# Optimization experiments

Measured on AMD Instinct MI355X. Metric: run time of the kernel, lower is better.

## Reference

```python
import jax, jax.numpy as jnp
import numpy as np

N, E, R, B, DIN, H1, H2 = 50000, 1000000, 8, 30, 64, 64, 64


def setup_inputs() -> dict:
    key = jax.random.key(0)
    ks = jax.random.split(key, 12)
    node_features = jax.random.normal(ks[0], (N, DIN), dtype=jnp.float32)
    src = jax.random.randint(ks[1], (E,), 0, N)
    dst = jax.random.randint(ks[2], (E,), 0, N)
    edge_index = jnp.stack([src, dst]).astype(jnp.int64)
    edge_norm = jax.random.uniform(ks[3], (E,), dtype=jnp.float32)
    edge_type = jax.random.randint(ks[4], (E,), 0, R).astype(jnp.int64)
    s = 0.05  # param init scale
    basis = jax.random.normal(ks[5], (B, DIN, H1), dtype=jnp.float32) * s
    comp = jax.random.normal(ks[6], (R, B), dtype=jnp.float32) * s
    loop_weight = jax.random.normal(ks[7], (DIN, H1), dtype=jnp.float32) * s
    bias1 = jnp.zeros((H1,), dtype=jnp.float32)
    weight2 = jax.random.normal(ks[8], (H1, H2), dtype=jnp.float32) * s
    bias2 = jnp.zeros((H2,), dtype=jnp.float32)
    return dict(node_features=node_features, edge_index=edge_index,
                edge_norm=edge_norm, edge_type=edge_type, basis=basis,
                comp=comp, loop_weight=loop_weight, bias1=bias1,
                weight2=weight2, bias2=bias2)


def reference(node_features, edge_index, edge_norm, edge_type, basis, comp,
              loop_weight, bias1, weight2, bias2):
    n = node_features.shape[0]
    src, dst = edge_index[0], edge_index[1]

    # ---- RGCNConv (basis decomposition, sum aggregation, self-loop, bias) ----
    # relation weights from bases: [R, DIN, H1]
    Wrel = jnp.einsum('rb,bio->rio', comp, basis)
    # transform every node by every relation once: [N, R, H1]
    xr = jnp.einsum('ni,rio->nro', node_features, Wrel)
    # per-edge message via (src, edge_type) gather: [E, H1]
    msg = xr[src, edge_type]
    agg1 = jax.ops.segment_sum(msg, dst, num_segments=n)
    h = agg1 + node_features @ loop_weight + bias1

    # ---- GraphConv (symmetric 'both' normalization) ----
    ones = jnp.ones((src.shape[0],), dtype=h.dtype)
    deg_out = jnp.clip(jax.ops.segment_sum(ones, src, num_segments=n), 1.0, None)
    deg_in = jnp.clip(jax.ops.segment_sum(ones, dst, num_segments=n), 1.0, None)
    hs = h * jax.lax.rsqrt(deg_out)[:, None]
    agg2 = jax.ops.segment_sum(hs[src], dst, num_segments=n)
    agg2 = agg2 * jax.lax.rsqrt(deg_in)[:, None]
    out = agg2 @ weight2 + bias2
    return out
```

## Files before the change

### kernel.cpp

```cpp
#include <hip/hip_runtime.h>

#define N_NODES 50000
#define N_EDGES 1000000
#define NB      128
#define CHUNK   7813
#define NQ      8
#define QN      6256
#define NBLK2   196

#define A_PART    0
#define A_XR      0
#define A_Y2      0
#define A_DEGP    115200000
#define A_ROWPTR  115400000
#define A_BSUM    115600128
#define A_BBASE   115601024
#define A_CSR     115601920
#define A_HS      123601920
#define A_WALL    136401920

typedef unsigned int uint32;

__global__ void k_wall(const float* __restrict__ comp, const float* __restrict__ basis,
                       const float* __restrict__ loopw, float* __restrict__ Wall) {
    int idx = blockIdx.x * 256 + threadIdx.x;
    if (idx >= 9 * 4096) return;
    int r = idx >> 12, io = idx & 4095;
    float acc;
    if (r < 8) {
        acc = 0.f;
        #pragma unroll
        for (int b = 0; b < 30; ++b) acc += comp[r * 30 + b] * basis[b * 4096 + io];
    } else {
        acc = loopw[io];
    }
    Wall[idx] = acc;
}

__global__ __launch_bounds__(256) void k_hist2(const int* __restrict__ ei,
                                               uint32* __restrict__ part) {
    __shared__ __align__(16) uint32 h[QN];
    int t = threadIdx.x, b = blockIdx.x, q = blockIdx.y;
    int lo = q * QN;
    int nq = N_NODES - lo; if (nq > QN) nq = QN;
    int4* h4 = (int4*)h;
    for (int i = t; i < QN / 4; i += 256) h4[i] = make_int4(0, 0, 0, 0);
    __syncthreads();
    int e0 = b * CHUNK, e1 = e0 + CHUNK;
    if (e1 > N_EDGES) e1 = N_EDGES;
    for (int e = e0 + t; e < e1; e += 256) {
        int s = ei[e], d = ei[N_EDGES + e];
        unsigned rs = (unsigned)(s - lo), rd = (unsigned)(d - lo);
        if (rs < (unsigned)QN) atomicAdd(&h[rs], 1u);
        if (rd < (unsigned)QN) atomicAdd(&h[rd], 0x10000u);
    }
    __syncthreads();
    int4* d4 = (int4*)(part + b * N_NODES + lo);
    const int4* s4 = (const int4*)h;
    for (int i = t; i < nq / 4; i += 256) d4[i] = s4[i];
}

__global__ __launch_bounds__(256) void k_merge(const uint32* __restrict__ part,
                                               uint32* __restrict__ degp,
                                               int* __restrict__ bsum) {
    int t = threadIdx.x, v = blockIdx.x * 256 + t;
    uint32 s = 0;
    if (v < N_NODES) {
        #pragma unroll 8
        for (int b = 0; b < NB; ++b) s += part[b * N_NODES + v];
        degp[v] = s;
    }
    int din = (int)(s >> 16);
    int r = din;
    #pragma unroll
    for (int d = 1; d < 64; d <<= 1) r += __shfl_xor(r, d);
    __shared__ int wsum[4];
    int lane = t & 63, wid = t >> 6;
    if (lane == 0) wsum[wid] = r;
    __syncthreads();
    if (t == 0) bsum[blockIdx.x] = wsum[0] + wsum[1] + wsum[2] + wsum[3];
}

__global__ void k_scanb(const int* __restrict__ bsum, int* __restrict__ bbase) {
    int t = threadIdx.x;
    int v = (t < NBLK2) ? bsum[t] : 0;
    int lane = t & 63, wid = t >> 6;
    int x = v;
    #pragma unroll
    for (int d = 1; d < 64; d <<= 1) {
        int y = __shfl_up(x, d);
        if (lane >= d) x += y;
    }
    __shared__ int wsum[4];
    if (lane == 63) wsum[wid] = x;
    __syncthreads();
    int base = 0;
    for (int w = 0; w < wid; ++w) base += wsum[w];
    if (t < NBLK2) bbase[t] = base + x - v;
}

__global__ __launch_bounds__(256) void k_base(uint32* __restrict__ part,
                                              const uint32* __restrict__ degp,
                                              const int* __restrict__ bbase,
                                              int* __restrict__ rowptr) {
    int t = threadIdx.x, v = blockIdx.x * 256 + t;
    int din = (v < N_NODES) ? (int)(degp[v] >> 16) : 0;
    int lane = t & 63, wid = t >> 6;
    int x = din;
    #pragma unroll
    for (int d = 1; d < 64; d <<= 1) {
        int y = __shfl_up(x, d);
        if (lane >= d) x += y;
    }
    __shared__ int wsum[4];
    if (lane == 63) wsum[wid] = x;
    __syncthreads();
    int base = bbase[blockIdx.x];
    for (int w = 0; w < wid; ++w) base += wsum[w];
    int start = base + x - din;
    if (v < N_NODES) {
        rowptr[v] = start;
        if (v == N_NODES - 1) rowptr[N_NODES] = start + din;
        uint32 run = (uint32)start;
        for (int b = 0; b < NB; ++b) {
            uint32 p = part[b * N_NODES + v];
            part[b * N_NODES + v] = run;
            run += (p >> 16);
        }
    }
}

__global__ __launch_bounds__(256) void k_fill2(const int* __restrict__ ei,
                                               const int* __restrict__ etype,
                                               const uint32* __restrict__ fillbase,
                                               int2* __restrict__ csr) {
    __shared__ __align__(16) uint32 cur[QN];
    int t = threadIdx.x, b = blockIdx.x, q = blockIdx.y;
    int lo = q * QN;
    int nq = N_NODES - lo; if (nq > QN) nq = QN;
    const int4* s4 = (const int4*)(fillbase + b * N_NODES + lo);
    int4* c4 = (int4*)cur;
    for (int i = t; i < nq / 4; i += 256) c4[i] = s4[i];
    __syncthreads();
    int e0 = b * CHUNK, e1 = e0 + CHUNK;
    if (e1 > N_EDGES) e1 = N_EDGES;
    for (int e = e0 + t; e < e1; e += 256) {
        int d = ei[N_EDGES + e];
        unsigned rd = (unsigned)(d - lo);
        if (rd < (unsigned)QN) {
            int s = ei[e], ty = etype[e];
            uint32 pos = atomicAdd(&cur[rd], 1u);
            csr[pos] = make_int2(s * 9 + ty, s);
        }
    }
}

__global__ __launch_bounds__(256) void k_xr(const float* __restrict__ x,
                                            const float* __restrict__ Wall,
                                            float* __restrict__ xr) {
    __shared__ __align__(16) float At[32 * 256];
    __shared__ __align__(16) float Wt[32 * 64];
    int t = threadIdx.x;
    int n0 = blockIdx.x * 256;
    int r = blockIdx.y;
    int og = t & 7, ng = t >> 3;
    float acc[8][8];
    #pragma unroll
    for (int i = 0; i < 8; ++i)
        #pragma unroll
        for (int j = 0; j < 8; ++j) acc[i][j] = 0.f;

    #pragma unroll
    for (int ph = 0; ph < 2; ++ph) {
        if (ph) __syncthreads();
        #pragma unroll
        for (int j = 0; j < 8; ++j) {
            int f4 = t + j * 256;
            int n = f4 >> 3, k4 = f4 & 7;
            float4 v = make_float4(0.f, 0.f, 0.f, 0.f);
            if (n0 + n < N_NODES)
                v = *(const float4*)&x[(n0 + n) * 64 + ph * 32 + k4 * 4];
            int sl = n >> 2, nl = n & 3, kb = k4 * 4;
            At[(kb + 0) * 256 + (((sl ^ ((kb + 0) & 7)) << 2) | nl)] = v.x;
            At[(kb + 1) * 256 + (((sl ^ ((kb + 1) & 7)) << 2) | nl)] = v.y;
            At[(kb + 2) * 256 + (((sl ^ ((kb + 2) & 7)) << 2) | nl)] = v.z;
            At[(kb + 3) * 256 + (((sl ^ ((kb + 3) & 7)) << 2) | nl)] = v.w;
        }
        #pragma unroll
        for (int j = 0; j < 8; ++j) {
            int f = t + j * 256;
            Wt[f] = Wall[r * 4096 + ph * 2048 + f];
        }
        __syncthreads();
        #pragma unroll 4
        for (int k = 0; k < 32; ++k) {
            int c = k & 7;
            float4 aA = *(const float4*)&At[k * 256 + (((2 * ng) ^ c) << 2)];
            float4 aB = *(const float4*)&At[k * 256 + (((2 * ng + 1) ^ c) << 2)];
            float4 w0 = *(const float4*)&Wt[k * 64 + og * 8];
            float4 w1 = *(const float4*)&Wt[k * 64 + og * 8 + 4];
            float a_[8] = {aA.x, aA.y, aA.z, aA.w, aB.x, aB.y, aB.z, aB.w};
            float w_[8] = {w0.x, w0.y, w0.z, w0.w, w1.x, w1.y, w1.z, w1.w};
            #pragma unroll
            for (int i = 0; i < 8; ++i)
                #pragma unroll
                for (int j = 0; j < 8; ++j) acc[i][j] += a_[i] * w_[j];
        }
    }
    #pragma unroll
    for (int i = 0; i < 8; ++i) {
        int n = n0 + ng * 8 + i;
        if (n < N_NODES) {
            *(float4*)&xr[n * 576 + r * 64 + og * 8] =
                make_float4(acc[i][0], acc[i][1], acc[i][2], acc[i][3]);
            *(float4*)&xr[n * 576 + r * 64 + og * 8 + 4] =
                make_float4(acc[i][4], acc[i][5], acc[i][6], acc[i][7]);
        }
    }
}

__global__ __launch_bounds__(256) void k_agg1(const float* __restrict__ xr,
                                              const int2* __restrict__ csr,
                                              const int* __restrict__ rowptr,
                                              const uint32* __restrict__ degp,
                                              const float* __restrict__ bias1,
                                              float* __restrict__ hs) {
    int wid = threadIdx.x >> 6, lane = threadIdx.x & 63;
    int v = blockIdx.x * 4 + wid;
    if (v >= N_NODES) return;
    float acc = xr[(v * 9 + 8) * 64 + lane] + bias1[lane];
    int j = rowptr[v], end = rowptr[v + 1];
    for (; j + 4 <= end; j += 4) {
        int r0 = csr[j].x, r1 = csr[j + 1].x, r2 = csr[j + 2].x, r3 = csr[j + 3].x;
        float a0 = xr[r0 * 64 + lane], a1 = xr[r1 * 64 + lane];
        float a2 = xr[r2 * 64 + lane], a3 = xr[r3 * 64 + lane];
        acc += a0; acc += a1; acc += a2; acc += a3;
    }
    for (; j < end; ++j) acc += xr[csr[j].x * 64 + lane];
    float dg = (float)(degp[v] & 0xffffu);
    if (dg < 1.f) dg = 1.f;
    hs[v * 64 + lane] = acc * rsqrtf(dg);
}

__global__ __launch_bounds__(256) void k_agg2(const float* __restrict__ hs,
                                              const int2* __restrict__ csr,
                                              const int* __restrict__ rowptr,
                                              const uint32* __restrict__ degp,
                                              float* __restrict__ y2) {
    int wid = threadIdx.x >> 6, lane = threadIdx.x & 63;
    int v = blockIdx.x * 4 + wid;
    if (v >= N_NODES) return;
    float acc = 0.f;
    int j = rowptr[v], end = rowptr[v + 1];
    for (; j + 4 <= end; j += 4) {
        int r0 = csr[j].y, r1 = csr[j + 1].y, r2 = csr[j + 2].y, r3 = csr[j + 3].y;
        float a0 = hs[r0 * 64 + lane], a1 = hs[r1 * 64 + lane];
        float a2 = hs[r2 * 64 + lane], a3 = hs[r3 * 64 + lane];
        acc += a0; acc += a1; acc += a2; acc += a3;
    }
    for (; j < end; ++j) acc += hs[csr[j].y * 64 + lane];
    float dg = (float)(degp[v] >> 16);
    if (dg < 1.f) dg = 1.f;
    y2[v * 64 + lane] = acc * rsqrtf(dg);
}

__global__ __launch_bounds__(256) void k_gemm2(const float* __restrict__ y2,
                                               const float* __restrict__ w2,
                                               const float* __restrict__ bias2,
                                               float* __restrict__ out) {
    __shared__ __align__(16) float At[32 * 256];
    __shared__ __align__(16) float Wt[32 * 64];
    int t = threadIdx.x;
    int n0 = blockIdx.x * 256;
    int og = t & 7, ng = t >> 3;
    float acc[8][8];
    #pragma unroll
    for (int i = 0; i < 8; ++i)
        #pragma unroll
        for (int j = 0; j < 8; ++j) acc[i][j] = 0.f;

    #pragma unroll
    for (int ph = 0; ph < 2; ++ph) {
        if (ph) __syncthreads();
        #pragma unroll
        for (int j = 0; j < 8; ++j) {
            int f4 = t + j * 256;
            int n = f4 >> 3, k4 = f4 & 7;
            float4 v = make_float4(0.f, 0.f, 0.f, 0.f);
            if (n0 + n < N_NODES)
                v = *(const float4*)&y2[(n0 + n) * 64 + ph * 32 + k4 * 4];
            int sl = n >> 2, nl = n & 3, kb = k4 * 4;
            At[(kb + 0) * 256 + (((sl ^ ((kb + 0) & 7)) << 2) | nl)] = v.x;
            At[(kb + 1) * 256 + (((sl ^ ((kb + 1) & 7)) << 2) | nl)] = v.y;
            At[(kb + 2) * 256 + (((sl ^ ((kb + 2) & 7)) << 2) | nl)] = v.z;
            At[(kb + 3) * 256 + (((sl ^ ((kb + 3) & 7)) << 2) | nl)] = v.w;
        }
        #pragma unroll
        for (int j = 0; j < 8; ++j) {
            int f = t + j * 256;
            Wt[f] = w2[ph * 2048 + f];
        }
        __syncthreads();
        #pragma unroll 4
        for (int k = 0; k < 32; ++k) {
            int c = k & 7;
            float4 aA = *(const float4*)&At[k * 256 + (((2 * ng) ^ c) << 2)];
            float4 aB = *(const float4*)&At[k * 256 + (((2 * ng + 1) ^ c) << 2)];
            float4 w0 = *(const float4*)&Wt[k * 64 + og * 8];
            float4 w1 = *(const float4*)&Wt[k * 64 + og * 8 + 4];
            float a_[8] = {aA.x, aA.y, aA.z, aA.w, aB.x, aB.y, aB.z, aB.w};
            float w_[8] = {w0.x, w0.y, w0.z, w0.w, w1.x, w1.y, w1.z, w1.w};
            #pragma unroll
            for (int i = 0; i < 8; ++i)
                #pragma unroll
                for (int j = 0; j < 8; ++j) acc[i][j] += a_[i] * w_[j];
        }
    }
    float4 b0 = *(const float4*)&bias2[og * 8];
    float4 b1 = *(const float4*)&bias2[og * 8 + 4];
    #pragma unroll
    for (int i = 0; i < 8; ++i) {
        int n = n0 + ng * 8 + i;
        if (n < N_NODES) {
            *(float4*)&out[n * 64 + og * 8] =
                make_float4(acc[i][0] + b0.x, acc[i][1] + b0.y,
                            acc[i][2] + b0.z, acc[i][3] + b0.w);
            *(float4*)&out[n * 64 + og * 8 + 4] =
                make_float4(acc[i][4] + b1.x, acc[i][5] + b1.y,
                            acc[i][6] + b1.z, acc[i][7] + b1.w);
        }
    }
}

extern "C" void kernel_launch(void* const* d_in, const int* in_sizes, int n_in,
                              void* d_out, int out_size, void* d_ws, size_t ws_size,
                              hipStream_t stream) {
    const float* x      = (const float*)d_in[0];
    const int*   ei     = (const int*)d_in[1];
    const int*   etype  = (const int*)d_in[3];
    const float* basis  = (const float*)d_in[4];
    const float* comp   = (const float*)d_in[5];
    const float* loopw  = (const float*)d_in[6];
    const float* bias1  = (const float*)d_in[7];
    const float* w2     = (const float*)d_in[8];
    const float* bias2  = (const float*)d_in[9];
    float* out = (float*)d_out;

    char* ws = (char*)d_ws;
    uint32* part   = (uint32*)(ws + A_PART);
    float*  xr     = (float*)(ws + A_XR);
    float*  y2     = (float*)(ws + A_Y2);
    uint32* degp   = (uint32*)(ws + A_DEGP);
    int*    rowptr = (int*)(ws + A_ROWPTR);
    int*    bsum   = (int*)(ws + A_BSUM);
    int*    bbase  = (int*)(ws + A_BBASE);
    int2*   csr    = (int2*)(ws + A_CSR);
    float*  hs     = (float*)(ws + A_HS);
    float*  Wall   = (float*)(ws + A_WALL);

    k_wall<<<144, 256, 0, stream>>>(comp, basis, loopw, Wall);
    k_hist2<<<dim3(NB, NQ), 256, 0, stream>>>(ei, part);
    k_merge<<<NBLK2, 256, 0, stream>>>(part, degp, bsum);
    k_scanb<<<1, 256, 0, stream>>>(bsum, bbase);
    k_base<<<NBLK2, 256, 0, stream>>>(part, degp, bbase, rowptr);
    k_fill2<<<dim3(NB, NQ), 256, 0, stream>>>(ei, etype, part, csr);
    k_xr<<<dim3((N_NODES + 255) / 256, 9), 256, 0, stream>>>(x, Wall, xr);
    k_agg1<<<N_NODES / 4, 256, 0, stream>>>(xr, csr, rowptr, degp, bias1, hs);
    k_agg2<<<N_NODES / 4, 256, 0, stream>>>(hs, csr, rowptr, degp, y2);
    k_gemm2<<<(N_NODES + 255) / 256, 256, 0, stream>>>(y2, w2, bias2, out);
}
```

Baseline: 310.1 us.

## Replace partitioned LDS histogram CSR build with global-atomic counting and fill

The previous CSR build ran 128x8 blocks, each histogramming one edge chunk per node quarter in LDS, then merged and prefix-scanned 128 partial histograms per node. It now zeroes a degree array, counts degrees with one global atomic per edge endpoint, and fills the CSR with a global atomic cursor per destination node. This removes the eightfold re-reading of edges and the 128-way partial merge and scan traffic. In exchange it relies on contended global atomics, and the order of edges within each CSR row becomes nondeterministic, which changes the float summation order.

Result: slower. 417.9 us (+34.8%).

```diff
diff --git a/kernel.cpp b/kernel.cpp
--- a/kernel.cpp
+++ b/kernel.cpp
@@ -2,13 +2,10 @@
 
 #define N_NODES 50000
 #define N_EDGES 1000000
-#define NB      128
-#define CHUNK   7813
-#define NQ      8
-#define QN      6256
 #define NBLK2   196
-
-#define A_PART    0
+#define EBLK    3907
+
+#define A_CUR     0
 #define A_XR      0
 #define A_Y2      0
 #define A_DEGP    115200000
@@ -37,40 +34,23 @@
     Wall[idx] = acc;
 }
 
-__global__ __launch_bounds__(256) void k_hist2(const int* __restrict__ ei,
-                                               uint32* __restrict__ part) {
-    __shared__ __align__(16) uint32 h[QN];
-    int t = threadIdx.x, b = blockIdx.x, q = blockIdx.y;
-    int lo = q * QN;
-    int nq = N_NODES - lo; if (nq > QN) nq = QN;
-    int4* h4 = (int4*)h;
-    for (int i = t; i < QN / 4; i += 256) h4[i] = make_int4(0, 0, 0, 0);
-    __syncthreads();
-    int e0 = b * CHUNK, e1 = e0 + CHUNK;
-    if (e1 > N_EDGES) e1 = N_EDGES;
-    for (int e = e0 + t; e < e1; e += 256) {
-        int s = ei[e], d = ei[N_EDGES + e];
-        unsigned rs = (unsigned)(s - lo), rd = (unsigned)(d - lo);
-        if (rs < (unsigned)QN) atomicAdd(&h[rs], 1u);
-        if (rd < (unsigned)QN) atomicAdd(&h[rd], 0x10000u);
-    }
-    __syncthreads();
-    int4* d4 = (int4*)(part + b * N_NODES + lo);
-    const int4* s4 = (const int4*)h;
-    for (int i = t; i < nq / 4; i += 256) d4[i] = s4[i];
-}
-
-__global__ __launch_bounds__(256) void k_merge(const uint32* __restrict__ part,
-                                               uint32* __restrict__ degp,
-                                               int* __restrict__ bsum) {
+__global__ __launch_bounds__(256) void k_zero(uint32* __restrict__ degp) {
+    int v = blockIdx.x * 256 + threadIdx.x;
+    if (v < N_NODES) degp[v] = 0;
+}
+
+__global__ __launch_bounds__(256) void k_count(const int* __restrict__ ei,
+                                               uint32* __restrict__ degp) {
+    int e = blockIdx.x * 256 + threadIdx.x;
+    if (e >= N_EDGES) return;
+    atomicAdd(&degp[ei[e]], 1u);
+    atomicAdd(&degp[ei[N_EDGES + e]], 0x10000u);
+}
+
+__global__ __launch_bounds__(256) void k_bsum(const uint32* __restrict__ degp,
+                                              int* __restrict__ bsum) {
     int t = threadIdx.x, v = blockIdx.x * 256 + t;
-    uint32 s = 0;
-    if (v < N_NODES) {
-        #pragma unroll 8
-        for (int b = 0; b < NB; ++b) s += part[b * N_NODES + v];
-        degp[v] = s;
-    }
-    int din = (int)(s >> 16);
+    int din = (v < N_NODES) ? (int)(degp[v] >> 16) : 0;
     int r = din;
     #pragma unroll
     for (int d = 1; d < 64; d <<= 1) r += __shfl_xor(r, d);
@@ -99,10 +79,10 @@
     if (t < NBLK2) bbase[t] = base + x - v;
 }
 
-__global__ __launch_bounds__(256) void k_base(uint32* __restrict__ part,
-                                              const uint32* __restrict__ degp,
-                                              const int* __restrict__ bbase,
-                                              int* __restrict__ rowptr) {
+__global__ __launch_bounds__(256) void k_rowptr(const uint32* __restrict__ degp,
+                                                const int* __restrict__ bbase,
+                                                int* __restrict__ rowptr,
+                                                uint32* __restrict__ cur) {
     int t = threadIdx.x, v = blockIdx.x * 256 + t;
     int din = (v < N_NODES) ? (int)(degp[v] >> 16) : 0;
     int lane = t & 63, wid = t >> 6;
@@ -120,39 +100,20 @@
     int start = base + x - din;
     if (v < N_NODES) {
         rowptr[v] = start;
+        cur[v] = (uint32)start;
         if (v == N_NODES - 1) rowptr[N_NODES] = start + din;
-        uint32 run = (uint32)start;
-        for (int b = 0; b < NB; ++b) {
-            uint32 p = part[b * N_NODES + v];
-            part[b * N_NODES + v] = run;
-            run += (p >> 16);
-        }
-    }
-}
-
-__global__ __launch_bounds__(256) void k_fill2(const int* __restrict__ ei,
+    }
+}
+
+__global__ __launch_bounds__(256) void k_fill3(const int* __restrict__ ei,
                                                const int* __restrict__ etype,
-                                               const uint32* __restrict__ fillbase,
+                                               uint32* __restrict__ cur,
                                                int2* __restrict__ csr) {
-    __shared__ __align__(16) uint32 cur[QN];
-    int t = threadIdx.x, b = blockIdx.x, q = blockIdx.y;
-    int lo = q * QN;
-    int nq = N_NODES - lo; if (nq > QN) nq = QN;
-    const int4* s4 = (const int4*)(fillbase + b * N_NODES + lo);
-    int4* c4 = (int4*)cur;
-    for (int i = t; i < nq / 4; i += 256) c4[i] = s4[i];
-    __syncthreads();
-    int e0 = b * CHUNK, e1 = e0 + CHUNK;
-    if (e1 > N_EDGES) e1 = N_EDGES;
-    for (int e = e0 + t; e < e1; e += 256) {
-        int d = ei[N_EDGES + e];
-        unsigned rd = (unsigned)(d - lo);
-        if (rd < (unsigned)QN) {
-            int s = ei[e], ty = etype[e];
-            uint32 pos = atomicAdd(&cur[rd], 1u);
-            csr[pos] = make_int2(s * 9 + ty, s);
-        }
-    }
+    int e = blockIdx.x * 256 + threadIdx.x;
+    if (e >= N_EDGES) return;
+    int s = ei[e], d = ei[N_EDGES + e], ty = etype[e];
+    uint32 pos = atomicAdd(&cur[d], 1u);
+    csr[pos] = make_int2(s * 9 + ty, s);
 }
 
 __global__ __launch_bounds__(256) void k_xr(const float* __restrict__ x,
@@ -347,7 +308,7 @@
     float* out = (float*)d_out;
 
     char* ws = (char*)d_ws;
-    uint32* part   = (uint32*)(ws + A_PART);
+    uint32* cur    = (uint32*)(ws + A_CUR);
     float*  xr     = (float*)(ws + A_XR);
     float*  y2     = (float*)(ws + A_Y2);
     uint32* degp   = (uint32*)(ws + A_DEGP);
@@ -359,11 +320,12 @@
     float*  Wall   = (float*)(ws + A_WALL);
 
     k_wall<<<144, 256, 0, stream>>>(comp, basis, loopw, Wall);
-    k_hist2<<<dim3(NB, NQ), 256, 0, stream>>>(ei, part);
-    k_merge<<<NBLK2, 256, 0, stream>>>(part, degp, bsum);
+    k_zero<<<NBLK2, 256, 0, stream>>>(degp);
+    k_count<<<EBLK, 256, 0, stream>>>(ei, degp);
+    k_bsum<<<NBLK2, 256, 0, stream>>>(degp, bsum);
     k_scanb<<<1, 256, 0, stream>>>(bsum, bbase);
-    k_base<<<NBLK2, 256, 0, stream>>>(part, degp, bbase, rowptr);
-    k_fill2<<<dim3(NB, NQ), 256, 0, stream>>>(ei, etype, part, csr);
+    k_rowptr<<<NBLK2, 256, 0, stream>>>(degp, bbase, rowptr, cur);
+    k_fill3<<<EBLK, 256, 0, stream>>>(ei, etype, cur, csr);
     k_xr<<<dim3((N_NODES + 255) / 256, 9), 256, 0, stream>>>(x, Wall, xr);
     k_agg1<<<N_NODES / 4, 256, 0, stream>>>(xr, csr, rowptr, degp, bias1, hs);
     k_agg2<<<N_NODES / 4, 256, 0, stream>>>(hs, csr, rowptr, degp, y2);
```
